# Performance work log

Measured on AMD Instinct MI355X. Metric: run time of the kernel, lower is better.

## Reference

```python
import jax, jax.numpy as jnp
import numpy as np

C = 512
H_HEADS = 8
HEAD_DIM = C // H_HEADS


def setup_inputs() -> dict:
    key = jax.random.key(0)
    ks = jax.random.split(key, 6)
    B, Hs, Ws = 16, 32, 32
    x = jax.random.normal(ks[0], (B, C, Hs, Ws), dtype=jnp.float32)
    qkv_w = jax.random.normal(ks[1], (3 * C, C), dtype=jnp.float32) * 0.02
    proj_w = jax.random.normal(ks[2], (C, C), dtype=jnp.float32) * 0.02
    proj_b = jnp.zeros((C,), dtype=jnp.float32)
    ln_g = jnp.ones((C,), dtype=jnp.float32)
    ln_b = jnp.zeros((C,), dtype=jnp.float32)
    return {"x": x, "qkv_w": qkv_w, "proj_w": proj_w, "proj_b": proj_b,
            "ln_g": ln_g, "ln_b": ln_b}


def _layernorm(x, g, b, eps=1e-5):
    mu = jnp.mean(x, axis=-1, keepdims=True)
    var = jnp.var(x, axis=-1, keepdims=True)
    return (x - mu) * jax.lax.rsqrt(var + eps) * g + b


def reference(x, qkv_w, proj_w, proj_b, ln_g, ln_b):
    B, Cc, Hs, Ws = x.shape
    N = Hs * Ws
    # (B, N, C)
    x_flat = x.reshape(B, Cc, N).transpose(0, 2, 1)
    x_norm = _layernorm(x_flat, ln_g, ln_b)
    # qkv: torch Linear y = x @ W^T
    qkv = x_norm @ qkv_w.T  # (B, N, 3C)
    qkv = qkv.reshape(B, N, 3, H_HEADS, HEAD_DIM).transpose(2, 0, 3, 1, 4)
    q, k, v = qkv[0], qkv[1], qkv[2]  # (B, h, N, d)
    scale = HEAD_DIM ** -0.5
    attn = jnp.einsum('bhnd,bhmd->bhnm', q, k) * scale
    attn = jax.nn.softmax(attn, axis=-1)
    out = jnp.einsum('bhnm,bhmd->bhnd', attn, v)  # (B, h, N, d)
    out = out.transpose(0, 2, 1, 3).reshape(B, N, Cc)
    out = out @ proj_w.T + proj_b
    out = out + x_flat
    return out.transpose(0, 2, 1).reshape(B, Cc, Hs, Ws)
```

## Files before the change

kernel.cpp:

```cpp
#include <hip/hip_runtime.h>
#include <stdint.h>

typedef unsigned short u16;
typedef __attribute__((ext_vector_type(4))) float f32x4;
typedef __attribute__((ext_vector_type(8))) short s16x8;
typedef __attribute__((ext_vector_type(4))) unsigned short u16x4;
typedef __attribute__((ext_vector_type(8))) unsigned short u16x8;
typedef __attribute__((ext_vector_type(4))) unsigned int u32x4;

__device__ __forceinline__ u16 f2bf(float f) {
  union { float f; uint32_t u; } v; v.f = f;
  uint32_t r = (v.u + 0x7FFFu + ((v.u >> 16) & 1u)) >> 16;
  return (u16)r;
}

__device__ __forceinline__ uint32_t cvtpk(float lo, float hi) {
  uint32_t r;
  asm("v_cvt_pk_bf16_f32 %0, %1, %2" : "=v"(r) : "v"(lo), "v"(hi));
  return r;
}

__device__ __forceinline__ void gload_lds16(const void* g, void* l) {
  __builtin_amdgcn_global_load_lds((const __attribute__((address_space(1))) uint32_t*)g,
                                   (__attribute__((address_space(3))) uint32_t*)l, 16, 0, 0);
}

__global__ __launch_bounds__(256) void cvt_kernel(const float* __restrict__ src,
                                                  u16* __restrict__ dst, int n) {
  const int i = (blockIdx.x * 256 + threadIdx.x) * 4;
  if (i < n) {
    f32x4 v = *(const f32x4*)(src + i);
    u16x4 p;
    p[0] = f2bf(v[0]); p[1] = f2bf(v[1]); p[2] = f2bf(v[2]); p[3] = f2bf(v[3]);
    *(u16x4*)(dst + i) = p;
  }
}

__global__ __launch_bounds__(256) void ln_kernel(const float* __restrict__ x,
                                                 const float* __restrict__ lng,
                                                 const float* __restrict__ lnb,
                                                 u16* __restrict__ xn) {
  __shared__ float xt[16][516];
  __shared__ float ps[16][16], pq[16][16];
  __shared__ float smu[16], srs[16];
  const int tid = threadIdx.x;
  const int tok0 = blockIdx.x << 4;
  const int b = tok0 >> 10;
  const int nb = tok0 & 1023;
  const float* xb = x + (size_t)b * 512 * 1024 + nb;
  {
    const int n4 = (tid & 3) * 4;
    const int cr = tid >> 2;
#pragma unroll
    for (int it = 0; it < 8; ++it) {
      const int c = it * 64 + cr;
      f32x4 v = *(const f32x4*)(xb + (size_t)c * 1024 + n4);
      xt[n4 + 0][c] = v[0]; xt[n4 + 1][c] = v[1];
      xt[n4 + 2][c] = v[2]; xt[n4 + 3][c] = v[3];
    }
  }
  __syncthreads();
  {
    const int n = tid & 15, part = tid >> 4;
    float s = 0.f, q = 0.f;
#pragma unroll
    for (int i = 0; i < 8; ++i) {
      f32x4 v = *(const f32x4*)&xt[n][part * 32 + i * 4];
#pragma unroll
      for (int j = 0; j < 4; ++j) { s += v[j]; q += v[j] * v[j]; }
    }
    ps[part][n] = s; pq[part][n] = q;
  }
  __syncthreads();
  if (tid < 16) {
    float s = 0.f, q = 0.f;
#pragma unroll
    for (int p = 0; p < 16; ++p) { s += ps[p][tid]; q += pq[p][tid]; }
    const float mu = s * (1.f / 512.f);
    const float var = q * (1.f / 512.f) - mu * mu;
    smu[tid] = mu; srs[tid] = rsqrtf(var + 1e-5f);
  }
  __syncthreads();
  {
    const int n = tid >> 4, sub = tid & 15;
    const float mu = smu[n], rs = srs[n];
    u16* dst = xn + (size_t)(tok0 + n) * 512;
#pragma unroll
    for (int i = 0; i < 4; ++i) {
      const int c = (sub + 16 * i) * 8;
      f32x4 v0 = *(const f32x4*)&xt[n][c];
      f32x4 v1 = *(const f32x4*)&xt[n][c + 4];
      f32x4 g0 = *(const f32x4*)(lng + c);
      f32x4 g1 = *(const f32x4*)(lng + c + 4);
      f32x4 b0 = *(const f32x4*)(lnb + c);
      f32x4 b1 = *(const f32x4*)(lnb + c + 4);
      union { u32x4 w; u16x8 v; } pk;
      float r0 = (v0[0] - mu) * rs * g0[0] + b0[0];
      float r1 = (v0[1] - mu) * rs * g0[1] + b0[1];
      float r2 = (v0[2] - mu) * rs * g0[2] + b0[2];
      float r3 = (v0[3] - mu) * rs * g0[3] + b0[3];
      float r4 = (v1[0] - mu) * rs * g1[0] + b1[0];
      float r5 = (v1[1] - mu) * rs * g1[1] + b1[1];
      float r6 = (v1[2] - mu) * rs * g1[2] + b1[2];
      float r7 = (v1[3] - mu) * rs * g1[3] + b1[3];
      pk.w[0] = cvtpk(r0, r1); pk.w[1] = cvtpk(r2, r3);
      pk.w[2] = cvtpk(r4, r5); pk.w[3] = cvtpk(r6, r7);
      *(u16x8*)(dst + c) = pk.v;
    }
  }
}

template <int EPI>
__global__ __launch_bounds__(256) void gemm_bt(const u16* __restrict__ A,
                                               const u16* __restrict__ Bw,
                                               void* __restrict__ Cout,
                                               u16* __restrict__ vt,
                                               const float* __restrict__ bias,
                                               const float* __restrict__ resid,
                                               int M, int N, int K,
                                               long bsz, long csz, long rsz) {
  __shared__ u16 Al[128 * 32];
  __shared__ u16 Bl[128 * 32];
  const int tid = threadIdx.x;
  const int w = tid >> 6, lane = tid & 63;
  const int lg = lane >> 4, l15 = lane & 15;
  const int wr = w >> 1, wc = w & 1;
  const int m0 = blockIdx.x * 128, n0 = blockIdx.y * 128;
  const int z = blockIdx.z;
  const u16* Bz = Bw + (size_t)z * bsz;
  const float* Rz = (EPI == 1) ? resid + (size_t)z * rsz : nullptr;

  f32x4 acc[4][4];
#pragma unroll
  for (int i = 0; i < 4; ++i)
#pragma unroll
    for (int j = 0; j < 4; ++j) acc[i][j] = (f32x4){0.f, 0.f, 0.f, 0.f};

  const int sr = lane >> 2, sch = (lane & 3) * 8;
  for (int k0 = 0; k0 < K; k0 += 32) {
    __syncthreads();
#pragma unroll
    for (int i = 0; i < 2; ++i) {
      gload_lds16(A + (size_t)(m0 + w * 32 + i * 16 + sr) * K + k0 + sch,
                  &Al[(w * 32 + i * 16) * 32]);
      gload_lds16(Bz + (size_t)(n0 + w * 32 + i * 16 + sr) * K + k0 + sch,
                  &Bl[(w * 32 + i * 16) * 32]);
    }
    __syncthreads();
    s16x8 af[4], bfr[4];
#pragma unroll
    for (int mi = 0; mi < 4; ++mi)
      af[mi] = *(const s16x8*)&Al[(wr * 64 + mi * 16 + l15) * 32 + lg * 8];
#pragma unroll
    for (int ni = 0; ni < 4; ++ni)
      bfr[ni] = *(const s16x8*)&Bl[(wc * 64 + ni * 16 + l15) * 32 + lg * 8];
#pragma unroll
    for (int mi = 0; mi < 4; ++mi)
#pragma unroll
      for (int ni = 0; ni < 4; ++ni)
        acc[mi][ni] = __builtin_amdgcn_mfma_f32_16x16x32_bf16(af[mi], bfr[ni], acc[mi][ni], 0, 0, 0);
  }

  if (EPI == 0) {
    u16* C = (u16*)Cout;
    if (n0 < 1024) {
#pragma unroll
      for (int mi = 0; mi < 4; ++mi)
#pragma unroll
        for (int ni = 0; ni < 4; ++ni) {
          const int col = n0 + wc * 64 + ni * 16 + l15;
          const int row = m0 + wr * 64 + mi * 16 + lg * 4;
          const uint32_t w0 = cvtpk(acc[mi][ni][0], acc[mi][ni][1]);
          const uint32_t w1 = cvtpk(acc[mi][ni][2], acc[mi][ni][3]);
          C[(size_t)(row + 0) * 1024 + col] = (u16)w0;
          C[(size_t)(row + 1) * 1024 + col] = (u16)(w0 >> 16);
          C[(size_t)(row + 2) * 1024 + col] = (u16)w1;
          C[(size_t)(row + 3) * 1024 + col] = (u16)(w1 >> 16);
        }
    } else {
#pragma unroll
      for (int mi = 0; mi < 4; ++mi)
#pragma unroll
        for (int ni = 0; ni < 4; ++ni) {
          const int vcol = n0 - 1024 + wc * 64 + ni * 16 + l15;
          const int hh = vcol >> 6, d = vcol & 63;
          const int token = m0 + wr * 64 + mi * 16 + lg * 4;
          const int b = token >> 10, g15 = (token >> 6) & 15;
          const int p = 32 * (mi >> 1) + 8 * lg + 4 * (mi & 1);
          union { uint32_t w[2]; u16x4 v; } pk;
          pk.w[0] = cvtpk(acc[mi][ni][0], acc[mi][ni][1]);
          pk.w[1] = cvtpk(acc[mi][ni][2], acc[mi][ni][3]);
          *(u16x4*)&vt[(size_t)((b * 8 + hh) * 64 + d) * 1024 + g15 * 64 + p] = pk.v;
        }
    }
  } else {
    float* C = (float*)Cout + (size_t)z * csz;
#pragma unroll
    for (int mi = 0; mi < 4; ++mi)
#pragma unroll
      for (int ni = 0; ni < 4; ++ni) {
        const int col = n0 + wc * 64 + ni * 16 + l15;
#pragma unroll
        for (int r = 0; r < 4; ++r) {
          const int row = m0 + wr * 64 + mi * 16 + lg * 4 + r;
          C[(size_t)row * N + col] = acc[mi][ni][r] + bias[row] + Rz[(size_t)row * N + col];
        }
      }
  }
}

__global__ __launch_bounds__(256, 4) void attn_kernel(const u16* __restrict__ qk,
                                                      const u16* __restrict__ vt,
                                                      u16* __restrict__ ao) {
  __shared__ union {
    struct { u16 K[2][64 * 64]; u16 V[2][64 * 64]; } s;
    struct { float O[4][16][68]; float ls[4 * 32]; } e;
  } sm;
  const int tid = threadIdx.x;
  const int w = tid >> 6, lane = tid & 63;
  const int lg = lane >> 4, l15 = lane & 15;
  const int blk = blockIdx.x;
  const int qb = (blk >> 3) & 7;
  const int bh = (blk & 7) | ((blk >> 6) << 3);
  const int b = bh >> 3, h = bh & 7;
  const size_t qbase = (size_t)b * 1024 * 1024;
  const size_t vbase = (size_t)bh * 64 * 1024;
  const int qtok0 = qb * 128 + w * 32;

  s16x8 qf[2][2];
#pragma unroll
  for (int s = 0; s < 2; ++s)
#pragma unroll
    for (int qg = 0; qg < 2; ++qg)
      qf[s][qg] = *(const s16x8*)(qk + qbase + (size_t)(qtok0 + qg * 16 + l15) * 1024 +
                                  h * 64 + lg * 8 + 32 * s);

  f32x4 o[2][4];
#pragma unroll
  for (int qg = 0; qg < 2; ++qg)
#pragma unroll
    for (int db = 0; db < 4; ++db) o[qg][db] = (f32x4){0.f, 0.f, 0.f, 0.f};
  float lrun[2] = {0.f, 0.f};
  const float CE = 0.125f * 1.44269504f;

  const int srr = lane >> 3, sch = lane & 7;
  const int row0 = w * 16 + srr, row1 = row0 + 8;
  const u16* kp0 = qk + qbase + (size_t)row0 * 1024 + 512 + h * 64 + ((sch ^ (row0 & 7)) * 8);
  const u16* kp1 = qk + qbase + (size_t)row1 * 1024 + 512 + h * 64 + ((sch ^ (row1 & 7)) * 8);
  const u16* vp0 = vt + vbase + (size_t)row0 * 1024 + ((sch ^ (row0 & 7)) * 8);
  const u16* vp1 = vt + vbase + (size_t)row1 * 1024 + ((sch ^ (row1 & 7)) * 8);

  auto stage = [&](int buf) {
    gload_lds16(kp0, &sm.s.K[buf][(w * 16 + 0) * 64]);
    gload_lds16(kp1, &sm.s.K[buf][(w * 16 + 8) * 64]);
    gload_lds16(vp0, &sm.s.V[buf][(w * 16 + 0) * 64]);
    gload_lds16(vp1, &sm.s.V[buf][(w * 16 + 8) * 64]);
    kp0 += 64 * 1024; kp1 += 64 * 1024;
    vp0 += 64; vp1 += 64;
  };

  auto compute = [&](int buf) {
    f32x4 st[4][2];
#pragma unroll
    for (int kg = 0; kg < 4; ++kg)
#pragma unroll
      for (int qg = 0; qg < 2; ++qg) st[kg][qg] = (f32x4){0.f, 0.f, 0.f, 0.f};
    __builtin_amdgcn_s_setprio(1);
#pragma unroll
    for (int s = 0; s < 2; ++s)
#pragma unroll
      for (int kg = 0; kg < 4; ++kg) {
        const int row = kg * 16 + l15;
        s16x8 kf = *(const s16x8*)&sm.s.K[buf][row * 64 +
                                              ((lg * 8 + 32 * s) ^ ((row & 7) << 3))];
#pragma unroll
        for (int qg = 0; qg < 2; ++qg)
          st[kg][qg] = __builtin_amdgcn_mfma_f32_16x16x32_bf16(kf, qf[s][qg], st[kg][qg], 0, 0, 0);
      }
    __builtin_amdgcn_s_setprio(0);

    s16x8 pa[2][2];
#pragma unroll
    for (int qg = 0; qg < 2; ++qg) {
      float pv[16];
#pragma unroll
      for (int kg = 0; kg < 4; ++kg)
#pragma unroll
        for (int r = 0; r < 4; ++r)
          pv[kg * 4 + r] = exp2f(st[kg][qg][r] * CE);
      float s01 = 0.f, s23 = 0.f;
#pragma unroll
      for (int j = 0; j < 4; ++j) { s01 += pv[j] + pv[4 + j]; s23 += pv[8 + j] + pv[12 + j]; }
      lrun[qg] += s01 + s23;
#pragma unroll
      for (int kh = 0; kh < 2; ++kh) {
        union { u32x4 wd; s16x8 v; } pk;
        pk.wd[0] = cvtpk(pv[8 * kh + 0], pv[8 * kh + 1]);
        pk.wd[1] = cvtpk(pv[8 * kh + 2], pv[8 * kh + 3]);
        pk.wd[2] = cvtpk(pv[8 * kh + 4], pv[8 * kh + 5]);
        pk.wd[3] = cvtpk(pv[8 * kh + 6], pv[8 * kh + 7]);
        pa[qg][kh] = pk.v;
      }
    }

    __builtin_amdgcn_s_setprio(1);
#pragma unroll
    for (int kh = 0; kh < 2; ++kh)
#pragma unroll
      for (int db = 0; db < 4; ++db) {
        const int d = db * 16 + l15;
        s16x8 vf = *(const s16x8*)&sm.s.V[buf][d * 64 +
                                               ((kh * 32 + lg * 8) ^ ((d & 7) << 3))];
#pragma unroll
        for (int qg = 0; qg < 2; ++qg)
          o[qg][db] = __builtin_amdgcn_mfma_f32_16x16x32_bf16(pa[qg][kh], vf, o[qg][db], 0, 0, 0);
      }
    __builtin_amdgcn_s_setprio(0);
  };

  stage(0);
  int cur = 0;
#pragma unroll 1
  for (int t = 0; t < 15; ++t) {
    stage(cur ^ 1);
    asm volatile("s_waitcnt vmcnt(4)" ::: "memory");
    __builtin_amdgcn_s_barrier();
    asm volatile("" ::: "memory");
    compute(cur);
    asm volatile("" ::: "memory");
    __builtin_amdgcn_s_barrier();
    cur ^= 1;
  }
  asm volatile("s_waitcnt vmcnt(0)" ::: "memory");
  __builtin_amdgcn_s_barrier();
  asm volatile("" ::: "memory");
  compute(cur);

#pragma unroll
  for (int qg = 0; qg < 2; ++qg) {
    lrun[qg] += __shfl_xor(lrun[qg], 16);
    lrun[qg] += __shfl_xor(lrun[qg], 32);
  }

  __syncthreads();
  if (lane < 16) {
    sm.e.ls[w * 32 + lane] = lrun[0];
    sm.e.ls[w * 32 + 16 + lane] = lrun[1];
  }
#pragma unroll
  for (int half = 0; half < 2; ++half) {
#pragma unroll
    for (int db = 0; db < 4; ++db)
#pragma unroll
      for (int r = 0; r < 4; ++r)
        sm.e.O[w][lg * 4 + r][db * 16 + l15] = o[half][db][r];
    __syncthreads();
    {
      const int q = lane & 15, dh = lane >> 4;
      const float inv = 1.0f / sm.e.ls[w * 32 + half * 16 + q];
      u16* dst = ao + (size_t)(b * 1024 + qtok0 + half * 16 + q) * 512 + h * 64 + dh * 16;
      f32x4 v0 = *(const f32x4*)&sm.e.O[w][q][dh * 16 + 0];
      f32x4 v1 = *(const f32x4*)&sm.e.O[w][q][dh * 16 + 4];
      f32x4 v2 = *(const f32x4*)&sm.e.O[w][q][dh * 16 + 8];
      f32x4 v3 = *(const f32x4*)&sm.e.O[w][q][dh * 16 + 12];
      union { u32x4 wd; u16x8 v; } p0, p1;
      p0.wd[0] = cvtpk(v0[0] * inv, v0[1] * inv);
      p0.wd[1] = cvtpk(v0[2] * inv, v0[3] * inv);
      p0.wd[2] = cvtpk(v1[0] * inv, v1[1] * inv);
      p0.wd[3] = cvtpk(v1[2] * inv, v1[3] * inv);
      p1.wd[0] = cvtpk(v2[0] * inv, v2[1] * inv);
      p1.wd[1] = cvtpk(v2[2] * inv, v2[3] * inv);
      p1.wd[2] = cvtpk(v3[0] * inv, v3[1] * inv);
      p1.wd[3] = cvtpk(v3[2] * inv, v3[3] * inv);
      *(u16x8*)(dst + 0) = p0.v;
      *(u16x8*)(dst + 8) = p1.v;
    }
    __syncthreads();
  }
}

extern "C" void kernel_launch(void* const* d_in, const int* in_sizes, int n_in,
                              void* d_out, int out_size, void* d_ws, size_t ws_size,
                              hipStream_t stream) {
  const float* x      = (const float*)d_in[0];
  const float* qkv_w  = (const float*)d_in[1];
  const float* proj_w = (const float*)d_in[2];
  const float* proj_b = (const float*)d_in[3];
  const float* ln_g   = (const float*)d_in[4];
  const float* ln_b   = (const float*)d_in[5];
  float* out = (float*)d_out;

  char* ws = (char*)d_ws;
  u16* xn  = (u16*)ws;
  u16* qk  = (u16*)(ws + (size_t)16 * 1024 * 1024);
  u16* vt  = (u16*)(ws + (size_t)48 * 1024 * 1024);
  u16* ao  = (u16*)(ws + (size_t)64 * 1024 * 1024);
  u16* qw  = (u16*)(ws + (size_t)80 * 1024 * 1024);
  u16* pw  = qw + 1536 * 512;

  cvt_kernel<<<768, 256, 0, stream>>>(qkv_w, qw, 1536 * 512);
  cvt_kernel<<<256, 256, 0, stream>>>(proj_w, pw, 512 * 512);
  ln_kernel<<<1024, 256, 0, stream>>>(x, ln_g, ln_b, xn);
  gemm_bt<0><<<dim3(128, 12, 1), 256, 0, stream>>>(xn, qw, qk, vt, nullptr, nullptr,
                                                   16384, 1024, 512, 0, 0, 0);
  attn_kernel<<<1024, 256, 0, stream>>>(qk, vt, ao);
  gemm_bt<1><<<dim3(4, 8, 16), 256, 0, stream>>>(pw, ao, out, nullptr, proj_b, x,
                                                 512, 1024, 512,
                                                 (long)1024 * 512, (long)512 * 1024,
                                                 (long)512 * 1024);
}
```

Before: 239.4 us.

## Double-buffer GEMM loads, remap blocks, fold softmax scale into Q, MFMA row sums

The QKV/proj GEMM now double-buffers its LDS tiles with async global-to-LDS loads and explicit waitcnt/barriers, so the next K-slice loads while the current one is multiplied. The QKV GEMM also gets a 1D grid remapped by XCD so blocks sharing A rows run together. The softmax scale·log2e is folded into Q in the GEMM epilogue, and attention uses raw v_exp_f32. Softmax row sums are computed with an extra MFMA against a ones vector instead of VALU adds and shuffles. The attention loop is unrolled by two to drop the buffer-index variable. Row sums now come from bf16-rounded probabilities, and Q is rounded after scaling, which slightly changes numerics.

```diff
diff --git a/kernel.cpp b/kernel.cpp
--- a/kernel.cpp
+++ b/kernel.cpp
@@ -18,6 +18,14 @@
   uint32_t r;
   asm("v_cvt_pk_bf16_f32 %0, %1, %2" : "=v"(r) : "v"(lo), "v"(hi));
   return r;
+}
+
+__device__ __forceinline__ float fexp2(float x) {
+#if __has_builtin(__builtin_amdgcn_exp2f)
+  return __builtin_amdgcn_exp2f(x);
+#else
+  float r; asm("v_exp_f32 %0, %1" : "=v"(r) : "v"(x)); return r;
+#endif
 }
 
 __device__ __forceinline__ void gload_lds16(const void* g, void* l) {
@@ -119,14 +127,22 @@
                                                const float* __restrict__ resid,
                                                int M, int N, int K,
                                                long bsz, long csz, long rsz) {
-  __shared__ u16 Al[128 * 32];
-  __shared__ u16 Bl[128 * 32];
+  __shared__ u16 Al[2][128 * 32];
+  __shared__ u16 Bl[2][128 * 32];
   const int tid = threadIdx.x;
   const int w = tid >> 6, lane = tid & 63;
   const int lg = lane >> 4, l15 = lane & 15;
   const int wr = w >> 1, wc = w & 1;
-  const int m0 = blockIdx.x * 128, n0 = blockIdx.y * 128;
-  const int z = blockIdx.z;
+  int m0, n0, z;
+  if (EPI == 0) {
+    const int blk = blockIdx.x;
+    const int c = blk & 7, j = blk >> 3;
+    m0 = (c * 16 + j / 12) * 128;
+    n0 = (j % 12) * 128;
+    z = 0;
+  } else {
+    m0 = blockIdx.x * 128; n0 = blockIdx.y * 128; z = blockIdx.z;
+  }
   const u16* Bz = Bw + (size_t)z * bsz;
   const float* Rz = (EPI == 1) ? resid + (size_t)z * rsz : nullptr;
 
@@ -137,31 +153,72 @@
     for (int j = 0; j < 4; ++j) acc[i][j] = (f32x4){0.f, 0.f, 0.f, 0.f};
 
   const int sr = lane >> 2, sch = (lane & 3) * 8;
-  for (int k0 = 0; k0 < K; k0 += 32) {
-    __syncthreads();
-#pragma unroll
-    for (int i = 0; i < 2; ++i) {
-      gload_lds16(A + (size_t)(m0 + w * 32 + i * 16 + sr) * K + k0 + sch,
-                  &Al[(w * 32 + i * 16) * 32]);
-      gload_lds16(Bz + (size_t)(n0 + w * 32 + i * 16 + sr) * K + k0 + sch,
-                  &Bl[(w * 32 + i * 16) * 32]);
-    }
-    __syncthreads();
+  const u16* ap = A + (size_t)(m0 + w * 32 + sr) * K + sch;
+  const u16* bp = Bz + (size_t)(n0 + w * 32 + sr) * K + sch;
+
+  auto stage = [&](int buf) {
+    gload_lds16(ap,          &Al[buf][(w * 32 + 0) * 32]);
+    gload_lds16(ap + 16 * K, &Al[buf][(w * 32 + 16) * 32]);
+    gload_lds16(bp,          &Bl[buf][(w * 32 + 0) * 32]);
+    gload_lds16(bp + 16 * K, &Bl[buf][(w * 32 + 16) * 32]);
+    ap += 32; bp += 32;
+  };
+  auto compute = [&](int buf) {
     s16x8 af[4], bfr[4];
 #pragma unroll
     for (int mi = 0; mi < 4; ++mi)
-      af[mi] = *(const s16x8*)&Al[(wr * 64 + mi * 16 + l15) * 32 + lg * 8];
+      af[mi] = *(const s16x8*)&Al[buf][(wr * 64 + mi * 16 + l15) * 32 + lg * 8];
 #pragma unroll
     for (int ni = 0; ni < 4; ++ni)
-      bfr[ni] = *(const s16x8*)&Bl[(wc * 64 + ni * 16 + l15) * 32 + lg * 8];
+      bfr[ni] = *(const s16x8*)&Bl[buf][(wc * 64 + ni * 16 + l15) * 32 + lg * 8];
 #pragma unroll
     for (int mi = 0; mi < 4; ++mi)
 #pragma unroll
       for (int ni = 0; ni < 4; ++ni)
         acc[mi][ni] = __builtin_amdgcn_mfma_f32_16x16x32_bf16(af[mi], bfr[ni], acc[mi][ni], 0, 0, 0);
-  }
+  };
+
+  const int nk2 = K >> 6;
+  stage(0);
+#pragma unroll 1
+  for (int it = 0; it < nk2 - 1; ++it) {
+    stage(1);
+    asm volatile("s_waitcnt vmcnt(4)" ::: "memory");
+    __builtin_amdgcn_s_barrier();
+    asm volatile("" ::: "memory");
+    compute(0);
+    asm volatile("" ::: "memory");
+    __builtin_amdgcn_s_barrier();
+    stage(0);
+    asm volatile("s_waitcnt vmcnt(4)" ::: "memory");
+    __builtin_amdgcn_s_barrier();
+    asm volatile("" ::: "memory");
+    compute(1);
+    asm volatile("" ::: "memory");
+    __builtin_amdgcn_s_barrier();
+  }
+  stage(1);
+  asm volatile("s_waitcnt vmcnt(4)" ::: "memory");
+  __builtin_amdgcn_s_barrier();
+  asm volatile("" ::: "memory");
+  compute(0);
+  asm volatile("" ::: "memory");
+  __builtin_amdgcn_s_barrier();
+  asm volatile("s_waitcnt vmcnt(0)" ::: "memory");
+  __builtin_amdgcn_s_barrier();
+  asm volatile("" ::: "memory");
+  compute(1);
 
   if (EPI == 0) {
+    if (n0 < 512) {
+      const float ce = 0.125f * 1.44269504f;
+#pragma unroll
+      for (int mi = 0; mi < 4; ++mi)
+#pragma unroll
+        for (int ni = 0; ni < 4; ++ni)
+#pragma unroll
+          for (int r = 0; r < 4; ++r) acc[mi][ni][r] *= ce;
+    }
     u16* C = (u16*)Cout;
     if (n0 < 1024) {
 #pragma unroll
@@ -236,12 +293,16 @@
                                   h * 64 + lg * 8 + 32 * s);
 
   f32x4 o[2][4];
-#pragma unroll
-  for (int qg = 0; qg < 2; ++qg)
+  f32x4 lacc[2];
+#pragma unroll
+  for (int qg = 0; qg < 2; ++qg) {
+    lacc[qg] = (f32x4){0.f, 0.f, 0.f, 0.f};
 #pragma unroll
     for (int db = 0; db < 4; ++db) o[qg][db] = (f32x4){0.f, 0.f, 0.f, 0.f};
-  float lrun[2] = {0.f, 0.f};
-  const float CE = 0.125f * 1.44269504f;
+  }
+  s16x8 ones;
+#pragma unroll
+  for (int j = 0; j < 8; ++j) ones[j] = (short)0x3F80;
 
   const int srr = lane >> 3, sch = lane & 7;
   const int row0 = w * 16 + srr, row1 = row0 + 8;
@@ -287,11 +348,7 @@
       for (int kg = 0; kg < 4; ++kg)
 #pragma unroll
         for (int r = 0; r < 4; ++r)
-          pv[kg * 4 + r] = exp2f(st[kg][qg][r] * CE);
-      float s01 = 0.f, s23 = 0.f;
-#pragma unroll
-      for (int j = 0; j < 4; ++j) { s01 += pv[j] + pv[4 + j]; s23 += pv[8 + j] + pv[12 + j]; }
-      lrun[qg] += s01 + s23;
+          pv[kg * 4 + r] = fexp2(st[kg][qg][r]);
 #pragma unroll
       for (int kh = 0; kh < 2; ++kh) {
         union { u32x4 wd; s16x8 v; } pk;
@@ -305,7 +362,7 @@
 
     __builtin_amdgcn_s_setprio(1);
 #pragma unroll
-    for (int kh = 0; kh < 2; ++kh)
+    for (int kh = 0; kh < 2; ++kh) {
 #pragma unroll
       for (int db = 0; db < 4; ++db) {
         const int d = db * 16 + l15;
@@ -315,37 +372,50 @@
         for (int qg = 0; qg < 2; ++qg)
           o[qg][db] = __builtin_amdgcn_mfma_f32_16x16x32_bf16(pa[qg][kh], vf, o[qg][db], 0, 0, 0);
       }
+#pragma unroll
+      for (int qg = 0; qg < 2; ++qg)
+        lacc[qg] = __builtin_amdgcn_mfma_f32_16x16x32_bf16(pa[qg][kh], ones, lacc[qg], 0, 0, 0);
+    }
     __builtin_amdgcn_s_setprio(0);
   };
 
   stage(0);
-  int cur = 0;
 #pragma unroll 1
-  for (int t = 0; t < 15; ++t) {
-    stage(cur ^ 1);
+  for (int it = 0; it < 7; ++it) {
+    stage(1);
     asm volatile("s_waitcnt vmcnt(4)" ::: "memory");
     __builtin_amdgcn_s_barrier();
     asm volatile("" ::: "memory");
-    compute(cur);
-    asm volatile("" ::: "memory");
-    __builtin_amdgcn_s_barrier();
-    cur ^= 1;
-  }
+    compute(0);
+    asm volatile("" ::: "memory");
+    __builtin_amdgcn_s_barrier();
+    stage(0);
+    asm volatile("s_waitcnt vmcnt(4)" ::: "memory");
+    __builtin_amdgcn_s_barrier();
+    asm volatile("" ::: "memory");
+    compute(1);
+    asm volatile("" ::: "memory");
+    __builtin_amdgcn_s_barrier();
+  }
+  stage(1);
+  asm volatile("s_waitcnt vmcnt(4)" ::: "memory");
+  __builtin_amdgcn_s_barrier();
+  asm volatile("" ::: "memory");
+  compute(0);
+  asm volatile("" ::: "memory");
+  __builtin_amdgcn_s_barrier();
   asm volatile("s_waitcnt vmcnt(0)" ::: "memory");
   __builtin_amdgcn_s_barrier();
   asm volatile("" ::: "memory");
-  compute(cur);
-
-#pragma unroll
-  for (int qg = 0; qg < 2; ++qg) {
-    lrun[qg] += __shfl_xor(lrun[qg], 16);
-    lrun[qg] += __shfl_xor(lrun[qg], 32);
-  }
+  compute(1);
 
   __syncthreads();
-  if (lane < 16) {
-    sm.e.ls[w * 32 + lane] = lrun[0];
-    sm.e.ls[w * 32 + 16 + lane] = lrun[1];
+  if (l15 == 0) {
+#pragma unroll
+    for (int qg = 0; qg < 2; ++qg)
+#pragma unroll
+      for (int r = 0; r < 4; ++r)
+        sm.e.ls[w * 32 + qg * 16 + lg * 4 + r] = lacc[qg][r];
   }
 #pragma unroll
   for (int half = 0; half < 2; ++half) {
@@ -401,8 +471,8 @@
   cvt_kernel<<<768, 256, 0, stream>>>(qkv_w, qw, 1536 * 512);
   cvt_kernel<<<256, 256, 0, stream>>>(proj_w, pw, 512 * 512);
   ln_kernel<<<1024, 256, 0, stream>>>(x, ln_g, ln_b, xn);
-  gemm_bt<0><<<dim3(128, 12, 1), 256, 0, stream>>>(xn, qw, qk, vt, nullptr, nullptr,
-                                                   16384, 1024, 512, 0, 0, 0);
+  gemm_bt<0><<<1536, 256, 0, stream>>>(xn, qw, qk, vt, nullptr, nullptr,
+                                       16384, 1024, 512, 0, 0, 0);
   attn_kernel<<<1024, 256, 0, stream>>>(qk, vt, ao);
   gemm_bt<1><<<dim3(4, 8, 16), 256, 0, stream>>>(pw, ao, out, nullptr, proj_b, x,
                                                  512, 1024, 512,
```

Result: faster. 222.8 us (-6.9%).
